# Kernel tuning notes

Measured on AMD Instinct MI355X. Metric: run time of the kernel, lower is better.

## Reference

```python
import jax, jax.numpy as jnp
import numpy as np

LOG2PI = float(np.log(2.0 * np.pi))
T, S, D, K = 1024, 512, 32, 64


def setup_inputs() -> dict:
    key = jax.random.key(0)
    k0, k1, k2, k3, k4 = jax.random.split(key, 5)
    data = jax.random.normal(k0, (T, S, D), dtype=jnp.float32)  # packed time-major
    ip = jax.random.uniform(k1, (K,), dtype=jnp.float32)
    initial_probs = ip / ip.sum()
    A = jax.random.uniform(k2, (K, K), dtype=jnp.float32)
    transition_probs = A / A.sum(-1, keepdims=True)  # row-stochastic
    means = jax.random.normal(k3, (K, D), dtype=jnp.float32)
    covars = jax.random.uniform(k4, (K, D), dtype=jnp.float32) * 0.5 + 0.5  # positive diag
    return {"data": data, "initial_probs": initial_probs,
            "transition_probs": transition_probs, "means": means, "covars": covars}


def _emission_probs(data, means, covars):
    # Gaussian diag-covariance densities, [T, S, K], without materializing [T,S,K,D].
    inv = 1.0 / covars  # [K, D]
    quad = (jnp.einsum('tsd,kd->tsk', data * data, inv)
            - 2.0 * jnp.einsum('tsd,kd->tsk', data, means * inv)
            + (means * means * inv).sum(-1))  # [T, S, K]
    logp = -0.5 * (quad + jnp.log(covars).sum(-1) + data.shape[-1] * LOG2PI)
    return jnp.exp(logp)


def reference(data, initial_probs, transition_probs, means, covars):
    probs = _emission_probs(data, means, covars)  # [T, S, K]
    # t = 0: alpha = normalize(initial * emission)
    a0 = initial_probs * probs[0]
    d0 = a0.sum(-1, keepdims=True)
    alpha0 = a0 / d0
    log_denom0 = jnp.log(d0)  # [S, 1]

    def step(carry, p_t):
        alpha, log_denom = carry
        a = p_t * (alpha @ transition_probs)  # [S, K]
        d = a.sum(-1, keepdims=True)
        return (a / d, log_denom + jnp.log(d)), None

    (alpha, log_denom), _ = jax.lax.scan(step, (alpha0, log_denom0), probs[1:])
    log_likeli = jax.nn.logsumexp(jnp.log(alpha) + log_denom, axis=-1).sum()
    return alpha, -log_likeli
```

## Files before the change

kernel.cpp:

```cpp
#include <hip/hip_runtime.h>
#include <hip/hip_fp16.h>
#include <math.h>

#define TT 1024
#define SS 512
#define DD 32
#define KK 64

#define LOG2PI_F 1.8378770664093453f

#define NSEG 4
#define SEGLEN (TT / NSEG)
#define BURN 64

#define PBUF_BYTES ((size_t)TT * SS * KK * 2)
#define EM_WPB 4
#define EM_BLOCKS 2048
#define NWAVES (EM_BLOCKS * EM_WPB)

typedef float v2f __attribute__((ext_vector_type(2)));

__device__ __forceinline__ v2f fma2(v2f a, v2f b, v2f c) {
#if __has_builtin(__builtin_elementwise_fma)
    return __builtin_elementwise_fma(a, b, c);
#else
    v2f r; r.x = fmaf(a.x, b.x, c.x); r.y = fmaf(a.y, b.y, c.y); return r;
#endif
}

template <int CTRL, int RMASK>
__device__ __forceinline__ float dpp_add(float x) {
    int t = __builtin_amdgcn_update_dpp(0, __float_as_int(x), CTRL, RMASK, 0xf, true);
    return x + __int_as_float(t);
}
template <int CTRL, int RMASK>
__device__ __forceinline__ float dpp_max(float x) {
    int xi = __float_as_int(x);
    int t = __builtin_amdgcn_update_dpp(xi, xi, CTRL, RMASK, 0xf, false);
    return fmaxf(x, __int_as_float(t));
}
__device__ __forceinline__ float wave_reduce_sum(float x) {
    x = dpp_add<0x111, 0xf>(x);
    x = dpp_add<0x112, 0xf>(x);
    x = dpp_add<0x114, 0xf>(x);
    x = dpp_add<0x118, 0xf>(x);
    x = dpp_add<0x142, 0xa>(x);
    x = dpp_add<0x143, 0xc>(x);
    return __int_as_float(__builtin_amdgcn_readlane(__float_as_int(x), 63));
}
__device__ __forceinline__ float wave_reduce_max(float x) {
    x = dpp_max<0x111, 0xf>(x);
    x = dpp_max<0x112, 0xf>(x);
    x = dpp_max<0x114, 0xf>(x);
    x = dpp_max<0x118, 0xf>(x);
    x = dpp_max<0x142, 0xa>(x);
    x = dpp_max<0x143, 0xc>(x);
    return __int_as_float(__builtin_amdgcn_readlane(__float_as_int(x), 63));
}

__global__ __launch_bounds__(EM_WPB * 64)
__attribute__((amdgpu_waves_per_eu(1, 2)))
void emission_kernel(
    const float* __restrict__ data,
    const float* __restrict__ means,
    const float* __restrict__ covars,
    __half* __restrict__ pbuf,
    float* __restrict__ mpart)
{
    const int k  = threadIdx.x & 63;
    const int w  = threadIdx.x >> 6;
    const int wv = blockIdx.x * EM_WPB + w;

    v2f w2[DD / 2], m2[DD / 2];
    float c0 = DD * LOG2PI_F;
#pragma unroll
    for (int d = 0; d < DD; ++d) {
        float c = covars[k * DD + d];
        ((float*)w2)[d] = 1.0f / c;
        ((float*)m2)[d] = means[k * DD + d];
        c0 += __logf(c);
    }

    __shared__ __align__(16) float4 xst[EM_WPB][2][64];

    const int base = wv * 64;
    const float4* dsrc = (const float4*)(data + (size_t)base * DD);

    float4 xr = dsrc[k];
    xst[w][0][k] = xr;
    __builtin_amdgcn_wave_barrier();

    float macc = 0.0f;
    int cur = 0;

    for (int b = 0; b < 8; ++b) {
        const int bn = (b + 1 < 8) ? (b + 1) : 7;
        xr = dsrc[bn * 64 + k];

        const float* xb = (const float*)&xst[w][cur][0];
#pragma unroll
        for (int i = 0; i < 8; ++i) {
            const int item = base + b * 8 + i;
            const float4* xq = (const float4*)(xb + i * DD);
            v2f q0 = {0.0f, 0.0f}, q1 = {0.0f, 0.0f};
#pragma unroll
            for (int d4 = 0; d4 < DD / 4; ++d4) {
                float4 x = xq[d4];
                v2f xa; xa.x = x.x; xa.y = x.y;
                v2f xb2; xb2.x = x.z; xb2.y = x.w;
                v2f ta = xa - m2[2 * d4];
                v2f tb = xb2 - m2[2 * d4 + 1];
                q0 = fma2(w2[2 * d4] * ta, ta, q0);
                q1 = fma2(w2[2 * d4 + 1] * tb, tb, q1);
            }
            float qq = (q0.x + q0.y) + (q1.x + q1.y);
            float logp = -0.5f * (qq + c0);
            float mx = wave_reduce_max(logp);
            pbuf[(size_t)item * KK + k] = __float2half(__expf(logp - mx));
            macc += mx;
        }

        xst[w][cur ^ 1][k] = xr;
        __builtin_amdgcn_wave_barrier();
        cur ^= 1;
    }
    if (k == 0) mpart[wv] = macc;
}

__global__ __launch_bounds__(64)
__attribute__((amdgpu_waves_per_eu(1, 2)))
void hmm_seq(
    const __half* __restrict__ pbuf,
    const float* __restrict__ initial,
    const float* __restrict__ trans,
    float* __restrict__ out_alpha,
    float* __restrict__ seq_logd)
{
    const int s   = blockIdx.x;
    const int seg = blockIdx.y;
    const int k   = threadIdx.x;

    const int emit_from = seg * SEGLEN;
    const int t0        = seg ? (emit_from - BURN) : 0;
    const int nsteps    = seg ? (SEGLEN + BURN) : SEGLEN;

    v2f acl[KK / 2];
#pragma unroll
    for (int j = 0; j < KK / 2; ++j) {
        acl[j].x = trans[(2 * j) * KK + k];
        acl[j].y = trans[(2 * j + 1) * KK + k];
    }

    __shared__ __align__(16) float alpha_sh[KK];

    const __half* pp = pbuf + (size_t)s * KK + k;
    const size_t PST = (size_t)SS * KK;

    __half pf[8];
#pragma unroll
    for (int i = 0; i < 8; ++i) pf[i] = pp[PST * (size_t)(t0 + i)];

    const float init_k = seg ? 1.0f : initial[k];
    float logd = 0.0f;
    float a = 0.0f;

    for (int mblk = 0; mblk < nsteps / 8; ++mblk) {
#pragma unroll
        for (int i = 0; i < 8; ++i) {
            const int t = t0 + 8 * mblk + i;
            const float pc = __half2float(pf[i]);
            int tn = t + 8; if (tn >= TT) tn = TT - 1;
            pf[i] = pp[PST * (size_t)tn];

            if (mblk == 0 && i == 0) {
                a = init_k * pc;
            } else {
                const float4* ash4 = (const float4*)alpha_sh;
                v2f a0 = {0,0}, a1 = {0,0}, a2 = {0,0}, a3 = {0,0};
#pragma unroll
                for (int j4 = 0; j4 < KK / 4; ++j4) {
                    float4 av = ash4[j4];
                    v2f lo; lo.x = av.x; lo.y = av.y;
                    v2f hi; hi.x = av.z; hi.y = av.w;
                    if (j4 & 1) {
                        a2 = fma2(lo, acl[2 * j4], a2);
                        a3 = fma2(hi, acl[2 * j4 + 1], a3);
                    } else {
                        a0 = fma2(lo, acl[2 * j4], a0);
                        a1 = fma2(hi, acl[2 * j4 + 1], a1);
                    }
                }
                v2f sv = (a0 + a1) + (a2 + a3);
                a = pc * (sv.x + sv.y);
            }

            if ((t & 3) == 3) {
                float den = wave_reduce_sum(a);
                logd += (t >= emit_from) ? __logf(den) : 0.0f;
                a *= __builtin_amdgcn_rcpf(den);
            }

            alpha_sh[k] = a;
            __builtin_amdgcn_wave_barrier();
        }
    }

    if (seg == NSEG - 1) out_alpha[(size_t)s * KK + k] = a;
    if (k == 0) seq_logd[seg * SS + s] = logd;
}

__global__ __launch_bounds__(256) void finalize(
    const float* __restrict__ seq_logd, const float* __restrict__ mpart,
    float* __restrict__ out_nll)
{
    float v = 0.0f;
    for (int j = threadIdx.x; j < NWAVES; j += 256) v += mpart[j];
    for (int j = threadIdx.x; j < NSEG * SS; j += 256) v += seq_logd[j];
#pragma unroll
    for (int off = 32; off > 0; off >>= 1)
        v += __shfl_xor(v, off, 64);
    __shared__ float sh[4];
    if ((threadIdx.x & 63) == 0) sh[threadIdx.x >> 6] = v;
    __syncthreads();
    if (threadIdx.x == 0) {
        double total = ((double)sh[0] + sh[1]) + ((double)sh[2] + sh[3]);
        out_nll[0] = (float)(-total);
    }
}

extern "C" void kernel_launch(void* const* d_in, const int* in_sizes, int n_in,
                              void* d_out, int out_size, void* d_ws, size_t ws_size,
                              hipStream_t stream) {
    const float* data    = (const float*)d_in[0];
    const float* initial = (const float*)d_in[1];
    const float* trans   = (const float*)d_in[2];
    const float* means   = (const float*)d_in[3];
    const float* covars  = (const float*)d_in[4];

    float* out_alpha = (float*)d_out;
    float* out_nll   = (float*)d_out + (size_t)SS * KK;

    __half* pbuf     = (__half*)d_ws;
    float*  mpart    = (float*)((char*)d_ws + PBUF_BYTES);
    float*  seq_logd = (float*)((char*)d_ws + PBUF_BYTES + NWAVES * sizeof(float));

    emission_kernel<<<EM_BLOCKS, EM_WPB * 64, 0, stream>>>(
        data, means, covars, pbuf, mpart);
    hmm_seq<<<dim3(SS, NSEG), 64, 0, stream>>>(
        pbuf, initial, trans, out_alpha, seq_logd);
    finalize<<<1, 256, 0, stream>>>(seq_logd, mpart, out_nll);
}
```

Baseline: 324.5 us.

## Double HMM segments, pair emission items for ILP, relax waves-per-EU hints

Raises the number of burn-in segments in the forward recursion from 4 to 8, so each sequence is split into shorter chains running in parallel. This cuts the serial step count per block but adds more redundant burn-in work. The emission kernel now computes two items at once and batches the eight wave max-reductions before the stores, to expose more instruction-level parallelism. Both kernels also get looser waves-per-EU occupancy hints.

```diff
diff --git a/kernel.cpp b/kernel.cpp
--- a/kernel.cpp
+++ b/kernel.cpp
@@ -9,7 +9,7 @@
 
 #define LOG2PI_F 1.8378770664093453f
 
-#define NSEG 4
+#define NSEG 8
 #define SEGLEN (TT / NSEG)
 #define BURN 64
 
@@ -59,7 +59,7 @@
 }
 
 __global__ __launch_bounds__(EM_WPB * 64)
-__attribute__((amdgpu_waves_per_eu(1, 2)))
+__attribute__((amdgpu_waves_per_eu(1, 3)))
 void emission_kernel(
     const float* __restrict__ data,
     const float* __restrict__ means,
@@ -93,42 +93,73 @@
     float macc = 0.0f;
     int cur = 0;
 
+#define QPAIR(I, LA, LB)                                                      \
+    {                                                                         \
+        const float4* x0q = (const float4*)(xb + (I) * DD);                   \
+        const float4* x1q = (const float4*)(xb + ((I) + 1) * DD);             \
+        v2f p00 = {0,0}, p01 = {0,0}, p10 = {0,0}, p11 = {0,0};               \
+        _Pragma("unroll")                                                     \
+        for (int d4 = 0; d4 < DD / 4; ++d4) {                                 \
+            float4 x0 = x0q[d4];                                              \
+            float4 x1 = x1q[d4];                                              \
+            v2f xa0; xa0.x = x0.x; xa0.y = x0.y;                              \
+            v2f xb0; xb0.x = x0.z; xb0.y = x0.w;                              \
+            v2f xa1; xa1.x = x1.x; xa1.y = x1.y;                              \
+            v2f xb1; xb1.x = x1.z; xb1.y = x1.w;                              \
+            v2f ta0 = xa0 - m2[2 * d4],  tb0 = xb0 - m2[2 * d4 + 1];          \
+            v2f ta1 = xa1 - m2[2 * d4],  tb1 = xb1 - m2[2 * d4 + 1];          \
+            p00 = fma2(w2[2 * d4] * ta0, ta0, p00);                           \
+            p01 = fma2(w2[2 * d4 + 1] * tb0, tb0, p01);                       \
+            p10 = fma2(w2[2 * d4] * ta1, ta1, p10);                           \
+            p11 = fma2(w2[2 * d4 + 1] * tb1, tb1, p11);                       \
+        }                                                                     \
+        v2f s0 = p00 + p01, s1 = p10 + p11;                                   \
+        LA = -0.5f * ((s0.x + s0.y) + c0);                                    \
+        LB = -0.5f * ((s1.x + s1.y) + c0);                                    \
+    }
+
     for (int b = 0; b < 8; ++b) {
         const int bn = (b + 1 < 8) ? (b + 1) : 7;
         xr = dsrc[bn * 64 + k];
 
         const float* xb = (const float*)&xst[w][cur][0];
-#pragma unroll
-        for (int i = 0; i < 8; ++i) {
-            const int item = base + b * 8 + i;
-            const float4* xq = (const float4*)(xb + i * DD);
-            v2f q0 = {0.0f, 0.0f}, q1 = {0.0f, 0.0f};
-#pragma unroll
-            for (int d4 = 0; d4 < DD / 4; ++d4) {
-                float4 x = xq[d4];
-                v2f xa; xa.x = x.x; xa.y = x.y;
-                v2f xb2; xb2.x = x.z; xb2.y = x.w;
-                v2f ta = xa - m2[2 * d4];
-                v2f tb = xb2 - m2[2 * d4 + 1];
-                q0 = fma2(w2[2 * d4] * ta, ta, q0);
-                q1 = fma2(w2[2 * d4 + 1] * tb, tb, q1);
-            }
-            float qq = (q0.x + q0.y) + (q1.x + q1.y);
-            float logp = -0.5f * (qq + c0);
-            float mx = wave_reduce_max(logp);
-            pbuf[(size_t)item * KK + k] = __float2half(__expf(logp - mx));
-            macc += mx;
-        }
+
+        float l0, l1, l2, l3, l4, l5, l6, l7;
+        QPAIR(0, l0, l1)
+        QPAIR(2, l2, l3)
+        QPAIR(4, l4, l5)
+        QPAIR(6, l6, l7)
+
+        float mx0 = wave_reduce_max(l0);
+        float mx1 = wave_reduce_max(l1);
+        float mx2 = wave_reduce_max(l2);
+        float mx3 = wave_reduce_max(l3);
+        float mx4 = wave_reduce_max(l4);
+        float mx5 = wave_reduce_max(l5);
+        float mx6 = wave_reduce_max(l6);
+        float mx7 = wave_reduce_max(l7);
+
+        __half* pb = pbuf + (size_t)(base + b * 8) * KK + k;
+        pb[0 * KK] = __float2half(__expf(l0 - mx0));
+        pb[1 * KK] = __float2half(__expf(l1 - mx1));
+        pb[2 * KK] = __float2half(__expf(l2 - mx2));
+        pb[3 * KK] = __float2half(__expf(l3 - mx3));
+        pb[4 * KK] = __float2half(__expf(l4 - mx4));
+        pb[5 * KK] = __float2half(__expf(l5 - mx5));
+        pb[6 * KK] = __float2half(__expf(l6 - mx6));
+        pb[7 * KK] = __float2half(__expf(l7 - mx7));
+        macc += ((mx0 + mx1) + (mx2 + mx3)) + ((mx4 + mx5) + (mx6 + mx7));
 
         xst[w][cur ^ 1][k] = xr;
         __builtin_amdgcn_wave_barrier();
         cur ^= 1;
     }
+#undef QPAIR
     if (k == 0) mpart[wv] = macc;
 }
 
 __global__ __launch_bounds__(64)
-__attribute__((amdgpu_waves_per_eu(1, 2)))
+__attribute__((amdgpu_waves_per_eu(1, 4)))
 void hmm_seq(
     const __half* __restrict__ pbuf,
     const float* __restrict__ initial,
```

Result: faster. 302.4 us (-6.8%).
